# Performance work log

Hardware: AMD Instinct MI355X
Metric: run time of the kernel (lower is better)

The kernel has to match this reference:

```python
import jax, jax.numpy as jnp
import numpy as np

B, N, M = 64, 4096, 128
TOTAL_LABELS = 21
TOTAL_POS = 128
TOTAL_NEG = 128
VARIANCES = jnp.array([0.1, 0.1, 0.2, 0.2], dtype=jnp.float32)


def _make_boxes(key, b, n):
    # valid [y1, x1, y2, x2] boxes in [0, 1]
    k1, k2 = jax.random.split(key)
    c1 = jax.random.uniform(k1, (b, n, 2), dtype=jnp.float32)
    c2 = jax.random.uniform(k2, (b, n, 2), dtype=jnp.float32)
    lo = jnp.minimum(c1, c2)
    hi = jnp.maximum(c1, c2)
    return jnp.concatenate([lo, hi], axis=-1)


def setup_inputs() -> dict:
    key = jax.random.key(0)
    k1, k2, k3 = jax.random.split(key, 3)
    roi_bboxes = _make_boxes(k1, B, N)
    gt_boxes = _make_boxes(k2, B, M)
    gt_labels = jax.random.randint(k3, (B, M), 0, TOTAL_LABELS, dtype=jnp.int32)
    return {"roi_bboxes": roi_bboxes, "gt_boxes": gt_boxes, "gt_labels": gt_labels}


def generate_iou(bboxes, gt_boxes):
    # bboxes: [B,N,4], gt_boxes: [B,M,4]; format [y1,x1,y2,x2] -> iou [B,N,M]
    by1, bx1, by2, bx2 = jnp.split(bboxes, 4, axis=-1)      # each [B,N,1]
    gy1, gx1, gy2, gx2 = jnp.split(gt_boxes, 4, axis=-1)    # each [B,M,1]
    gt_area = ((gy2 - gy1) * (gx2 - gx1))[..., 0]           # [B,M]
    bbox_area = ((by2 - by1) * (bx2 - bx1))[..., 0]         # [B,N]
    x_top = jnp.maximum(bx1, jnp.swapaxes(gx1, 1, 2))       # [B,N,M]
    y_top = jnp.maximum(by1, jnp.swapaxes(gy1, 1, 2))
    x_bot = jnp.minimum(bx2, jnp.swapaxes(gx2, 1, 2))
    y_bot = jnp.minimum(by2, jnp.swapaxes(gy2, 1, 2))
    inter = jnp.maximum(x_bot - x_top, 0.0) * jnp.maximum(y_bot - y_top, 0.0)
    union = bbox_area[:, :, None] + gt_area[:, None, :] - inter
    return inter / union


def randomly_select_mask(key, mask, count):
    # keep at most `count` True entries per row, chosen at random (rpn_utils.randomly_select_xyz_mask)
    rand = jax.random.randint(key, mask.shape, 1, count * 10, dtype=jnp.int32)
    mult = mask.astype(jnp.int32) * rand
    order = jnp.argsort(-mult, axis=1)       # descending sort of masked random scores
    rank = jnp.argsort(order, axis=1)        # rank of each element in that order
    return mask & (rank < count)


def bbox_to_delta(bboxes, gt_boxes):
    bw = bboxes[..., 3] - bboxes[..., 1]
    bh = bboxes[..., 2] - bboxes[..., 0]
    bcx = bboxes[..., 1] + 0.5 * bw
    bcy = bboxes[..., 0] + 0.5 * bh
    gw = gt_boxes[..., 3] - gt_boxes[..., 1]
    gh = gt_boxes[..., 2] - gt_boxes[..., 0]
    gcx = gt_boxes[..., 1] + 0.5 * gw
    gcy = gt_boxes[..., 0] + 0.5 * gh
    bw = jnp.where(bw == 0.0, 1e-3, bw)
    bh = jnp.where(bh == 0.0, 1e-3, bh)
    dx = (gcx - bcx) / bw
    dy = (gcy - bcy) / bh
    gw_safe = jnp.where(gw == 0.0, 1.0, gw)  # avoid nan grads through masked log
    gh_safe = jnp.where(gh == 0.0, 1.0, gh)
    dw = jnp.where(gw == 0.0, 0.0, jnp.log(gw_safe / bw))
    dh = jnp.where(gh == 0.0, 0.0, jnp.log(gh_safe / bh))
    return jnp.stack([dy, dx, dh, dw], axis=-1)


def _forward(roi_bboxes, gt_boxes, gt_labels):
    kp, kn = jax.random.split(jax.random.key(42))
    iou_map = generate_iou(roi_bboxes, gt_boxes)             # [B,N,M]
    max_idx = jnp.argmax(iou_map, axis=2)                    # [B,N]
    merged = jnp.max(iou_map, axis=2)                        # [B,N]
    pos_mask = randomly_select_mask(kp, merged > 0.5, TOTAL_POS)
    neg_mask = randomly_select_mask(kn, (merged < 0.5) & (merged > 0.1), TOTAL_NEG)
    # batched gather of best-matching gt box / label per roi
    gt_boxes_map = jnp.take_along_axis(gt_boxes, max_idx[..., None], axis=1)   # [B,N,4]
    gt_labels_map = jnp.take_along_axis(gt_labels, max_idx, axis=1)            # [B,N]
    expanded_gt_boxes = jnp.where(pos_mask[..., None], gt_boxes_map, 0.0)
    pos_gt_labels = jnp.where(pos_mask, gt_labels_map, -1)
    expanded_gt_labels = pos_gt_labels  # hyper_params['background'] == False
    deltas = bbox_to_delta(roi_bboxes, expanded_gt_boxes) / VARIANCES           # [B,N,4]
    labels_oh = jax.nn.one_hot(expanded_gt_labels, TOTAL_LABELS, dtype=deltas.dtype)  # [B,N,L]; -1 -> all zeros
    roi_bbox_deltas = labels_oh[..., None] * deltas[..., None, :]               # [B,N,L,4]
    return roi_bbox_deltas, labels_oh


def reference(roi_bboxes, gt_boxes, gt_labels):
    return _forward(roi_bboxes, gt_boxes, gt_labels)
```

## Files before the change

### kernel.cpp

```cpp
#include <hip/hip_runtime.h>
#include <stdint.h>

#pragma clang fp contract(off)


#define BB 64
#define NN 4096
#define MM 128
#define LL 21
#define NTOT (BB * NN)
#define DELTA_ELEMS ((size_t)BB * NN * LL * 4)

__host__ __device__ __forceinline__ uint32_t rotl32(uint32_t v, int s) {
  return (v << s) | (v >> (32 - s));
}

__host__ __device__ inline void threefry2x32(uint32_t k0, uint32_t k1,
                                             uint32_t x0, uint32_t x1,
                                             uint32_t* o0, uint32_t* o1) {
  const uint32_t ks2 = k0 ^ k1 ^ 0x1BD11BDAu;
  x0 += k0; x1 += k1;
#define TF_R(r) do { x0 += x1; x1 = rotl32(x1, (r)); x1 ^= x0; } while (0)
  TF_R(13); TF_R(15); TF_R(26); TF_R(6);
  x0 += k1;  x1 += ks2 + 1u;
  TF_R(17); TF_R(29); TF_R(16); TF_R(24);
  x0 += ks2; x1 += k0 + 2u;
  TF_R(13); TF_R(15); TF_R(26); TF_R(6);
  x0 += k0;  x1 += k1 + 3u;
  TF_R(17); TF_R(29); TF_R(16); TF_R(24);
  x0 += k1;  x1 += ks2 + 4u;
  TF_R(13); TF_R(15); TF_R(26); TF_R(6);
  x0 += ks2; x1 += k0 + 5u;
#undef TF_R
  *o0 = x0; *o1 = x1;
}

__device__ __forceinline__ uint32_t jax_bits32(uint32_t ka, uint32_t kb, uint32_t idx) {
  uint32_t o0, o1;
  threefry2x32(ka, kb, 0u, idx, &o0, &o1);
  return o0 ^ o1;
}

__device__ __forceinline__ uint32_t jax_randint_1_1280(uint32_t k1a, uint32_t k1b,
                                                       uint32_t k2a, uint32_t k2b,
                                                       uint32_t idx) {
  const uint32_t hi = jax_bits32(k1a, k1b, idx);
  const uint32_t lo = jax_bits32(k2a, k2b, idx);
  const uint32_t off = ((hi % 1279u) * 882u + (lo % 1279u)) % 1279u;
  return 1u + off;
}

__device__ __forceinline__ float4 compute_delta(const float4 r, const float4 g) {
  float bh = r.z - r.x, bw = r.w - r.y;
  const float bcy = r.x + 0.5f * bh, bcx = r.y + 0.5f * bw;
  const float gh = g.z - g.x, gw = g.w - g.y;
  const float gcy = g.x + 0.5f * gh, gcx = g.y + 0.5f * gw;
  if (bw == 0.0f) bw = 1e-3f;
  if (bh == 0.0f) bh = 1e-3f;
  const float dx = (gcx - bcx) / bw;
  const float dy = (gcy - bcy) / bh;
  const float dw = (gw == 0.0f) ? 0.0f : logf(gw / bw);
  const float dh = (gh == 0.0f) ? 0.0f : logf(gh / bh);
  float4 dv;
  dv.x = dy / 0.1f; dv.y = dx / 0.1f; dv.z = dh / 0.2f; dv.w = dw / 0.2f;
  return dv;
}

__global__ __launch_bounds__(256) void iou_pack_kernel(
    const float* __restrict__ roi, const float* __restrict__ gt,
    uint32_t* __restrict__ packed,
    uint32_t k1a, uint32_t k1b, uint32_t k2a, uint32_t k2b) {
  __shared__ float4 gtb[MM];
  const int b = blockIdx.y;
  const int t = threadIdx.x;
  const int i = b * NN + blockIdx.x * 256 + t;
  const float4 r = ((const float4*)roi)[i];
  if (t < MM) gtb[t] = ((const float4*)gt)[b * MM + t];
  __syncthreads();
  const float barea = (r.z - r.x) * (r.w - r.y);
  float best = -1.0f;
  int bm = 0;
  #pragma unroll 4
  for (int m = 0; m < MM; ++m) {
    const float4 g = gtb[m];
    const float garea = (g.z - g.x) * (g.w - g.y);
    const float xt = fmaxf(r.y, g.y);
    const float yt = fmaxf(r.x, g.x);
    const float xb = fminf(r.w, g.w);
    const float yb = fminf(r.z, g.z);
    const float inter = fmaxf(xb - xt, 0.0f) * fmaxf(yb - yt, 0.0f);
    const float iou = inter / ((barea + garea) - inter);
    if (iou > best) { best = iou; bm = m; }
  }
  const uint32_t rnd = jax_randint_1_1280(k1a, k1b, k2a, k2b, (uint32_t)i);
  packed[i] = (uint32_t)bm | ((best > 0.5f) ? (rnd << 7) : 0u);
}

__global__ __launch_bounds__(256) void fused_out_kernel(
    const float* __restrict__ roi, const float* __restrict__ gt,
    const int* __restrict__ glab, const uint32_t* __restrict__ packed,
    float* __restrict__ out) {
  __shared__ uint32_t hist[1280];
  __shared__ uint32_t scan[257];
  __shared__ uint32_t wsum[4];
  __shared__ unsigned char selb[NN];
  __shared__ float4 sdv[256];
  __shared__ int slbl[256];
  __shared__ int s_thr;
  __shared__ int s_take;
  const int br = blockIdx.x;
  const int b = br >> 4;
  const int win0 = (br & 15) << 8;
  const int t = threadIdx.x;
  const int lane = t & 63;
  const int wid = t >> 6;

  const int irow = win0 + t;
  const int i = b * NN + irow;
  const uint32_t pk_own = packed[i];
  const uint4* p4 = (const uint4*)(packed + (size_t)b * NN);
  const uint4 w0 = p4[t * 4 + 0];
  const uint4 w1 = p4[t * 4 + 1];
  const uint4 w2 = p4[t * 4 + 2];
  const uint4 w3 = p4[t * 4 + 3];
  const float4 r = ((const float4*)roi)[i];

  for (int j = t; j < 1280; j += 256) hist[j] = 0u;
  if (t == 0) { s_thr = 0; s_take = 0; scan[256] = 0u; }
  __syncthreads();

  uint32_t rv[16];
  rv[0] = w0.x >> 7;  rv[1] = w0.y >> 7;  rv[2] = w0.z >> 7;  rv[3] = w0.w >> 7;
  rv[4] = w1.x >> 7;  rv[5] = w1.y >> 7;  rv[6] = w1.z >> 7;  rv[7] = w1.w >> 7;
  rv[8] = w2.x >> 7;  rv[9] = w2.y >> 7;  rv[10] = w2.z >> 7; rv[11] = w2.w >> 7;
  rv[12] = w3.x >> 7; rv[13] = w3.y >> 7; rv[14] = w3.z >> 7; rv[15] = w3.w >> 7;
  #pragma unroll
  for (int k = 0; k < 16; ++k)
    if (rv[k]) atomicAdd(&hist[rv[k]], 1u);

  const int mi = (int)(pk_own & 127u);
  const float4 g = ((const float4*)gt)[b * MM + mi];
  int lbl = glab[b * MM + mi];
  float4 dv = compute_delta(r, g);
  __syncthreads();

  uint32_t chunk = 0;
  #pragma unroll
  for (int j = 0; j < 5; ++j) chunk += hist[t * 5 + j];
  uint32_t v = chunk;
  #pragma unroll
  for (int off = 1; off < 64; off <<= 1) {
    const uint32_t u = __shfl_down(v, off);
    if (lane + off < 64) v += u;
  }
  if (lane == 0) wsum[wid] = v;
  __syncthreads();
  {
    uint32_t add = 0;
    #pragma unroll
    for (int w = 0; w < 4; ++w)
      if (w > wid) add += wsum[w];
    v += add;
  }
  scan[t] = v;
  __syncthreads();
  const uint32_t total = scan[0];
  if (total > 128u) {
    const uint32_t Sc = v;
    const uint32_t Sn = scan[t + 1];
    if (Sc >= 128u && Sn < 128u) {
      uint32_t s = Sn;
      #pragma unroll
      for (int j = 4; j >= 0; --j) {
        const uint32_t h = hist[t * 5 + j];
        if (s + h >= 128u) { s_thr = t * 5 + j; s_take = 128 - (int)s; break; }
        s += h;
      }
    }
  }
  __syncthreads();
  const uint32_t thr = (uint32_t)s_thr;
  const uint32_t take = (uint32_t)s_take;

  uint32_t lt = 0;
  if (thr > 0) {
    #pragma unroll
    for (int k = 0; k < 16; ++k) lt += (rv[k] == thr) ? 1u : 0u;
  }
  uint32_t p = lt;
  #pragma unroll
  for (int off = 1; off < 64; off <<= 1) {
    const uint32_t u = __shfl_up(p, off);
    if (lane >= off) p += u;
  }
  if (lane == 63) wsum[wid] = p;
  __syncthreads();
  uint32_t run = p - lt;
  #pragma unroll
  for (int w = 0; w < 4; ++w)
    if (w < wid) run += wsum[w];

  uint32_t sw0 = 0, sw1 = 0, sw2 = 0, sw3 = 0;
  #pragma unroll
  for (int k = 0; k < 16; ++k) {
    bool s;
    if (thr == 0) {
      s = rv[k] > 0u;
    } else {
      s = (rv[k] > thr);
      if (rv[k] == thr) { s = (run < take); ++run; }
    }
    const uint32_t bit = s ? 1u : 0u;
    if (k < 4)       sw0 |= bit << (k * 8);
    else if (k < 8)  sw1 |= bit << ((k - 4) * 8);
    else if (k < 12) sw2 |= bit << ((k - 8) * 8);
    else             sw3 |= bit << ((k - 12) * 8);
  }
  ((uint4*)selb)[t] = make_uint4(sw0, sw1, sw2, sw3);
  __syncthreads();

  if (!selb[irow]) lbl = -1;
  sdv[t] = dv;
  slbl[t] = lbl;
  __syncthreads();
  const float4 z = {0.f, 0.f, 0.f, 0.f};
  const size_t ri0 = (size_t)b * NN + win0;
  float4* dbase = (float4*)out + ri0 * LL;
  #pragma unroll
  for (int k = 0; k < LL; ++k) {
    const int q = t + k * 256;
    const int rr = q / 21;
    const int f = q - rr * 21;
    dbase[q] = (f == slbl[rr]) ? sdv[rr] : z;
  }
  float4* lbase = (float4*)(out + DELTA_ELEMS) + ri0 * LL / 4;
  for (int q = t; q < 1344; q += 256) {
    const int e0 = q * 4;
    float4 vv;
    const int r0 = e0 / 21;       vv.x = ((e0 - r0 * 21) == slbl[r0]) ? 1.f : 0.f;
    const int r1 = (e0 + 1) / 21; vv.y = ((e0 + 1 - r1 * 21) == slbl[r1]) ? 1.f : 0.f;
    const int r2 = (e0 + 2) / 21; vv.z = ((e0 + 2 - r2 * 21) == slbl[r2]) ? 1.f : 0.f;
    const int r3 = (e0 + 3) / 21; vv.w = ((e0 + 3 - r3 * 21) == slbl[r3]) ? 1.f : 0.f;
    lbase[q] = vv;
  }
}

__global__ __launch_bounds__(256) void iou_kernel_s(const float* __restrict__ roi,
                                                    const float* __restrict__ gt,
                                                    int* __restrict__ midx,
                                                    float* __restrict__ merged) {
  __shared__ float4 gtb[MM];
  const int b = blockIdx.y;
  const int t = threadIdx.x;
  if (t < MM) gtb[t] = ((const float4*)gt)[b * MM + t];
  __syncthreads();
  const int i = b * NN + blockIdx.x * 256 + t;
  const float4 r = ((const float4*)roi)[i];
  const float barea = (r.z - r.x) * (r.w - r.y);
  float best = -1.0f;
  int bm = 0;
  for (int m = 0; m < MM; ++m) {
    const float4 g = gtb[m];
    const float garea = (g.z - g.x) * (g.w - g.y);
    const float xt = fmaxf(r.y, g.y);
    const float yt = fmaxf(r.x, g.x);
    const float xb = fminf(r.w, g.w);
    const float yb = fminf(r.z, g.z);
    const float inter = fmaxf(xb - xt, 0.0f) * fmaxf(yb - yt, 0.0f);
    const float iou = inter / ((barea + garea) - inter);
    if (iou > best) { best = iou; bm = m; }
  }
  midx[(size_t)i * 84] = bm;
  merged[(size_t)i * 84] = best;
}

__global__ __launch_bounds__(256) void select_kernel_s(const float* __restrict__ merged,
                                                       int* __restrict__ sel,
                                                       uint32_t k1a, uint32_t k1b,
                                                       uint32_t k2a, uint32_t k2b) {
  __shared__ uint32_t buf[NN];
  __shared__ uint32_t hist[1280];
  __shared__ uint32_t scan[256];
  __shared__ int s_thr;
  __shared__ int s_take;
  const int b = blockIdx.x;
  const int t = threadIdx.x;
  for (int j = t; j < 1280; j += 256) hist[j] = 0u;
  if (t == 0) { s_thr = 0; s_take = 0; }
  #pragma unroll
  for (int k = 0; k < 16; ++k) {
    const int li = t + k * 256;
    buf[li] = __float_as_uint(merged[(size_t)(b * NN + li) * 84]);
  }
  __syncthreads();
  uint32_t rv[16];
  const int lbase = t * 16;
  #pragma unroll
  for (int k = 0; k < 16; ++k) {
    const int li = lbase + k;
    uint32_t r = 0u;
    if (__uint_as_float(buf[li]) > 0.5f) {
      r = jax_randint_1_1280(k1a, k1b, k2a, k2b, (uint32_t)(b * NN + li));
      atomicAdd(&hist[r], 1u);
    }
    rv[k] = r;
  }
  __syncthreads();
  uint32_t chunk = 0;
  #pragma unroll
  for (int j = 0; j < 5; ++j) chunk += hist[t * 5 + j];
  scan[t] = chunk;
  __syncthreads();
  for (int off = 1; off < 256; off <<= 1) {
    const uint32_t v = (t + off < 256) ? scan[t + off] : 0u;
    __syncthreads();
    scan[t] += v;
    __syncthreads();
  }
  const uint32_t total = scan[0];
  if (total > 128u) {
    const uint32_t Sc = scan[t];
    const uint32_t Sn = (t < 255) ? scan[t + 1] : 0u;
    if (Sc >= 128u && Sn < 128u) {
      uint32_t s = Sn;
      #pragma unroll
      for (int j = 4; j >= 0; --j) {
        const uint32_t h = hist[t * 5 + j];
        if (s + h >= 128u) { s_thr = t * 5 + j; s_take = 128 - (int)s; break; }
        s += h;
      }
    }
  }
  __syncthreads();
  const int thr = s_thr;
  const uint32_t take = (uint32_t)s_take;
  uint32_t lt = 0;
  if (thr > 0) {
    #pragma unroll
    for (int k = 0; k < 16; ++k) lt += (rv[k] == (uint32_t)thr) ? 1u : 0u;
  }
  scan[t] = lt;
  __syncthreads();
  for (int off = 1; off < 256; off <<= 1) {
    const uint32_t v = (t >= off) ? scan[t - off] : 0u;
    __syncthreads();
    scan[t] += v;
    __syncthreads();
  }
  uint32_t run = scan[t] - lt;
  #pragma unroll
  for (int k = 0; k < 16; ++k) {
    bool s;
    if (thr == 0) {
      s = rv[k] > 0u;
    } else {
      s = (rv[k] > (uint32_t)thr);
      if (rv[k] == (uint32_t)thr) { s = (run < take); ++run; }
    }
    buf[lbase + k] = s ? 1u : 0u;
  }
  __syncthreads();
  #pragma unroll
  for (int k = 0; k < 16; ++k) {
    const int li = t + k * 256;
    sel[(size_t)(b * NN + li) * 84] = (int)buf[li];
  }
}

__global__ __launch_bounds__(256) void out_kernel_s(const float* __restrict__ roi,
                                                    const float* __restrict__ gt,
                                                    const int* __restrict__ glab,
                                                    const int* __restrict__ midx,
                                                    const int* __restrict__ sel,
                                                    float* __restrict__ out) {
  __shared__ float4 sdv[256];
  __shared__ int slbl[256];
  const int t = threadIdx.x;
  const int ri0 = blockIdx.x * 256;
  const int i = ri0 + t;
  const int b = i >> 12;
  const int mi = midx[(size_t)i * 84];
  const int sv = sel[(size_t)i * 84];
  float4 dv = {0.f, 0.f, 0.f, 0.f};
  int lbl = -1;
  if (sv) {
    const float4 r = ((const float4*)roi)[i];
    const float4 g = ((const float4*)gt)[b * MM + mi];
    lbl = glab[b * MM + mi];
    dv = compute_delta(r, g);
  }
  sdv[t] = dv;
  slbl[t] = lbl;
  __syncthreads();
  const float4 z = {0.f, 0.f, 0.f, 0.f};
  float4* dbase = (float4*)out + (size_t)ri0 * LL;
  #pragma unroll
  for (int k = 0; k < LL; ++k) {
    const int q = t + k * 256;
    const int r = q / 21;
    const int f = q - r * 21;
    dbase[q] = (f == slbl[r]) ? sdv[r] : z;
  }
  float4* lbase = (float4*)(out + DELTA_ELEMS) + (size_t)ri0 * LL / 4;
  for (int q = t; q < 1344; q += 256) {
    const int e0 = q * 4;
    float4 v;
    const int r0 = e0 / 21;       v.x = ((e0 - r0 * 21) == slbl[r0]) ? 1.f : 0.f;
    const int r1 = (e0 + 1) / 21; v.y = ((e0 + 1 - r1 * 21) == slbl[r1]) ? 1.f : 0.f;
    const int r2 = (e0 + 2) / 21; v.z = ((e0 + 2 - r2 * 21) == slbl[r2]) ? 1.f : 0.f;
    const int r3 = (e0 + 3) / 21; v.w = ((e0 + 3 - r3 * 21) == slbl[r3]) ? 1.f : 0.f;
    lbase[q] = v;
  }
}

extern "C" void kernel_launch(void* const* d_in, const int* in_sizes, int n_in,
                              void* d_out, int out_size, void* d_ws, size_t ws_size,
                              hipStream_t stream) {
  const float* roi = (const float*)d_in[0];
  const float* gt  = (const float*)d_in[1];
  const int* glab  = (const int*)d_in[2];
  float* out = (float*)d_out;

  uint32_t kp0, kp1, k1a, k1b, k2a, k2b;
  threefry2x32(0u, 42u, 0u, 0u, &kp0, &kp1);
  threefry2x32(kp0, kp1, 0u, 0u, &k1a, &k1b);
  threefry2x32(kp0, kp1, 0u, 1u, &k2a, &k2b);

  if (d_ws != nullptr && ws_size >= (size_t)NTOT * 4) {
    uint32_t* packed = (uint32_t*)d_ws;
    hipLaunchKernelGGL(iou_pack_kernel, dim3(NN / 256, BB), dim3(256), 0, stream,
                       roi, gt, packed, k1a, k1b, k2a, k2b);
    hipLaunchKernelGGL(fused_out_kernel, dim3(NTOT / 256), dim3(256), 0, stream,
                       roi, gt, glab, packed, out);
  } else {
    int* midx     = (int*)out;
    float* merged = out + 1;
    int* sel      = (int*)out + 2;
    hipLaunchKernelGGL(iou_kernel_s, dim3(NN / 256, BB), dim3(256), 0, stream,
                       roi, gt, midx, merged);
    hipLaunchKernelGGL(select_kernel_s, dim3(BB), dim3(256), 0, stream,
                       merged, sel, k1a, k1b, k2a, k2b);
    hipLaunchKernelGGL(out_kernel_s, dim3(NTOT / 256), dim3(256), 0, stream,
                       roi, gt, glab, midx, sel, out);
  }
}
```

Measured before the change: 57.58 us.

## Fuse IoU-pack and output kernels into one persistent kernel with grid barrier

Replaces the two-launch pipeline (IoU/pack kernel, then selection/output kernel) with a single 512-block kernel in which each thread processes two ROIs. Blocks synchronise through a software grid barrier built on an atomic counter in the workspace, so the packed per-batch scores are visible to all blocks before the histogram-based selection. Each block now covers 512 rows, which halves how many times the per-batch histogram and scan are recomputed, and removes the inter-kernel launch gap. It relies on all 512 blocks being co-resident (launch_bounds 256,2). The spin loop has a timeout guard that could silently break the barrier and produce wrong results if blocks are not all resident.

Measured after the change: 112.4 us. 1.95x slower.

```diff
diff --git a/kernel.cpp b/kernel.cpp
--- a/kernel.cpp
+++ b/kernel.cpp
@@ -10,6 +10,7 @@
 #define LL 21
 #define NTOT (BB * NN)
 #define DELTA_ELEMS ((size_t)BB * NN * LL * 4)
+#define NBLK 512
 
 __host__ __device__ __forceinline__ uint32_t rotl32(uint32_t v, int s) {
   return (v << s) | (v >> (32 - s));
@@ -66,64 +67,97 @@
   return dv;
 }
 
-__global__ __launch_bounds__(256) void iou_pack_kernel(
+__global__ __launch_bounds__(256, 2) void mega_kernel(
     const float* __restrict__ roi, const float* __restrict__ gt,
-    uint32_t* __restrict__ packed,
+    const int* __restrict__ glab, uint32_t* __restrict__ packed,
+    uint32_t* __restrict__ barA, const uint32_t* __restrict__ barB,
+    float* __restrict__ out,
     uint32_t k1a, uint32_t k1b, uint32_t k2a, uint32_t k2b) {
   __shared__ float4 gtb[MM];
-  const int b = blockIdx.y;
+  __shared__ uint32_t hist[1280];
+  __shared__ uint32_t scan[257];
+  __shared__ uint32_t wsum[4];
+  __shared__ unsigned char selb[512];
+  __shared__ float4 sdv[256];
+  __shared__ int slbl[256];
+  __shared__ int s_thr;
+  __shared__ int s_take;
+
+  const int br = blockIdx.x;
+  const int b = br >> 3;
+  const int wbase = (br & 7) << 9;
   const int t = threadIdx.x;
-  const int i = b * NN + blockIdx.x * 256 + t;
-  const float4 r = ((const float4*)roi)[i];
+  const int lane = t & 63;
+  const int wid = t >> 6;
+
+  const int i0 = b * NN + wbase + t;
+  const int i1 = i0 + 256;
+  const float4 r0 = ((const float4*)roi)[i0];
+  const float4 r1 = ((const float4*)roi)[i1];
   if (t < MM) gtb[t] = ((const float4*)gt)[b * MM + t];
   __syncthreads();
-  const float barea = (r.z - r.x) * (r.w - r.y);
-  float best = -1.0f;
-  int bm = 0;
+  const float ba0 = (r0.z - r0.x) * (r0.w - r0.y);
+  const float ba1 = (r1.z - r1.x) * (r1.w - r1.y);
+  float best0 = -1.0f, best1 = -1.0f;
+  int bm0 = 0, bm1 = 0;
   #pragma unroll 4
   for (int m = 0; m < MM; ++m) {
     const float4 g = gtb[m];
     const float garea = (g.z - g.x) * (g.w - g.y);
-    const float xt = fmaxf(r.y, g.y);
-    const float yt = fmaxf(r.x, g.x);
-    const float xb = fminf(r.w, g.w);
-    const float yb = fminf(r.z, g.z);
-    const float inter = fmaxf(xb - xt, 0.0f) * fmaxf(yb - yt, 0.0f);
-    const float iou = inter / ((barea + garea) - inter);
-    if (iou > best) { best = iou; bm = m; }
-  }
-  const uint32_t rnd = jax_randint_1_1280(k1a, k1b, k2a, k2b, (uint32_t)i);
-  packed[i] = (uint32_t)bm | ((best > 0.5f) ? (rnd << 7) : 0u);
-}
-
-__global__ __launch_bounds__(256) void fused_out_kernel(
-    const float* __restrict__ roi, const float* __restrict__ gt,
-    const int* __restrict__ glab, const uint32_t* __restrict__ packed,
-    float* __restrict__ out) {
-  __shared__ uint32_t hist[1280];
-  __shared__ uint32_t scan[257];
-  __shared__ uint32_t wsum[4];
-  __shared__ unsigned char selb[NN];
-  __shared__ float4 sdv[256];
-  __shared__ int slbl[256];
-  __shared__ int s_thr;
-  __shared__ int s_take;
-  const int br = blockIdx.x;
-  const int b = br >> 4;
-  const int win0 = (br & 15) << 8;
-  const int t = threadIdx.x;
-  const int lane = t & 63;
-  const int wid = t >> 6;
-
-  const int irow = win0 + t;
-  const int i = b * NN + irow;
-  const uint32_t pk_own = packed[i];
+    {
+      const float xt = fmaxf(r0.y, g.y);
+      const float yt = fmaxf(r0.x, g.x);
+      const float xb = fminf(r0.w, g.w);
+      const float yb = fminf(r0.z, g.z);
+      const float inter = fmaxf(xb - xt, 0.0f) * fmaxf(yb - yt, 0.0f);
+      const float iou = inter / ((ba0 + garea) - inter);
+      if (iou > best0) { best0 = iou; bm0 = m; }
+    }
+    {
+      const float xt = fmaxf(r1.y, g.y);
+      const float yt = fmaxf(r1.x, g.x);
+      const float xb = fminf(r1.w, g.w);
+      const float yb = fminf(r1.z, g.z);
+      const float inter = fmaxf(xb - xt, 0.0f) * fmaxf(yb - yt, 0.0f);
+      const float iou = inter / ((ba1 + garea) - inter);
+      if (iou > best1) { best1 = iou; bm1 = m; }
+    }
+  }
+  const uint32_t rnd0 = jax_randint_1_1280(k1a, k1b, k2a, k2b, (uint32_t)i0);
+  const uint32_t rnd1 = jax_randint_1_1280(k1a, k1b, k2a, k2b, (uint32_t)i1);
+  const uint32_t pk0 = (uint32_t)bm0 | ((best0 > 0.5f) ? (rnd0 << 7) : 0u);
+  const uint32_t pk1 = (uint32_t)bm1 | ((best1 > 0.5f) ? (rnd1 << 7) : 0u);
+  packed[i0] = pk0;
+  packed[i1] = pk1;
+
+  __syncthreads();
+  if (t == 0) {
+    const uint32_t base = __hip_atomic_load((uint32_t*)barB, __ATOMIC_RELAXED,
+                                            __HIP_MEMORY_SCOPE_AGENT);
+    const uint32_t old = __hip_atomic_fetch_add(barA, 1u, __ATOMIC_RELEASE,
+                                                __HIP_MEMORY_SCOPE_AGENT);
+    const uint32_t target = base + ((((old - base) >> 9) + 1u) << 9);
+    int guard = 0;
+    while ((int32_t)(__hip_atomic_load(barA, __ATOMIC_ACQUIRE,
+                                       __HIP_MEMORY_SCOPE_AGENT) - target) < 0) {
+      __builtin_amdgcn_s_sleep(2);
+      if (++guard > (1 << 21)) break;
+    }
+  }
+  __syncthreads();
+  __threadfence();
+
+  const int mi0 = (int)(pk0 & 127u);
+  const int mi1 = (int)(pk1 & 127u);
+  const int lbl0g = glab[b * MM + mi0];
+  const int lbl1g = glab[b * MM + mi1];
   const uint4* p4 = (const uint4*)(packed + (size_t)b * NN);
   const uint4 w0 = p4[t * 4 + 0];
   const uint4 w1 = p4[t * 4 + 1];
   const uint4 w2 = p4[t * 4 + 2];
   const uint4 w3 = p4[t * 4 + 3];
-  const float4 r = ((const float4*)roi)[i];
+  const float4 dv0 = compute_delta(r0, gtb[mi0]);
+  const float4 dv1 = compute_delta(r1, gtb[mi1]);
 
   for (int j = t; j < 1280; j += 256) hist[j] = 0u;
   if (t == 0) { s_thr = 0; s_take = 0; scan[256] = 0u; }
@@ -137,11 +171,6 @@
   #pragma unroll
   for (int k = 0; k < 16; ++k)
     if (rv[k]) atomicAdd(&hist[rv[k]], 1u);
-
-  const int mi = (int)(pk_own & 127u);
-  const float4 g = ((const float4*)gt)[b * MM + mi];
-  int lbl = glab[b * MM + mi];
-  float4 dv = compute_delta(r, g);
   __syncthreads();
 
   uint32_t chunk = 0;
@@ -200,7 +229,8 @@
   for (int w = 0; w < 4; ++w)
     if (w < wid) run += wsum[w];
 
-  uint32_t sw0 = 0, sw1 = 0, sw2 = 0, sw3 = 0;
+  const int ownerlo = wbase >> 4;
+  const bool owner = (t >= ownerlo) && (t < ownerlo + 32);
   #pragma unroll
   for (int k = 0; k < 16; ++k) {
     bool s;
@@ -210,38 +240,59 @@
       s = (rv[k] > thr);
       if (rv[k] == thr) { s = (run < take); ++run; }
     }
-    const uint32_t bit = s ? 1u : 0u;
-    if (k < 4)       sw0 |= bit << (k * 8);
-    else if (k < 8)  sw1 |= bit << ((k - 4) * 8);
-    else if (k < 12) sw2 |= bit << ((k - 8) * 8);
-    else             sw3 |= bit << ((k - 12) * 8);
-  }
-  ((uint4*)selb)[t] = make_uint4(sw0, sw1, sw2, sw3);
-  __syncthreads();
-
-  if (!selb[irow]) lbl = -1;
-  sdv[t] = dv;
-  slbl[t] = lbl;
-  __syncthreads();
+    if (owner) selb[(t - ownerlo) * 16 + k] = s ? 1 : 0;
+  }
+  __syncthreads();
+
   const float4 z = {0.f, 0.f, 0.f, 0.f};
-  const size_t ri0 = (size_t)b * NN + win0;
-  float4* dbase = (float4*)out + ri0 * LL;
-  #pragma unroll
-  for (int k = 0; k < LL; ++k) {
-    const int q = t + k * 256;
-    const int rr = q / 21;
-    const int f = q - rr * 21;
-    dbase[q] = (f == slbl[rr]) ? sdv[rr] : z;
-  }
-  float4* lbase = (float4*)(out + DELTA_ELEMS) + ri0 * LL / 4;
-  for (int q = t; q < 1344; q += 256) {
-    const int e0 = q * 4;
-    float4 vv;
-    const int r0 = e0 / 21;       vv.x = ((e0 - r0 * 21) == slbl[r0]) ? 1.f : 0.f;
-    const int r1 = (e0 + 1) / 21; vv.y = ((e0 + 1 - r1 * 21) == slbl[r1]) ? 1.f : 0.f;
-    const int r2 = (e0 + 2) / 21; vv.z = ((e0 + 2 - r2 * 21) == slbl[r2]) ? 1.f : 0.f;
-    const int r3 = (e0 + 3) / 21; vv.w = ((e0 + 3 - r3 * 21) == slbl[r3]) ? 1.f : 0.f;
-    lbase[q] = vv;
+  sdv[t] = dv0;
+  slbl[t] = selb[t] ? lbl0g : -1;
+  __syncthreads();
+  {
+    const size_t ri0 = (size_t)b * NN + wbase;
+    float4* dbase = (float4*)out + ri0 * LL;
+    #pragma unroll
+    for (int k = 0; k < LL; ++k) {
+      const int q = t + k * 256;
+      const int rr = q / 21;
+      const int f = q - rr * 21;
+      dbase[q] = (f == slbl[rr]) ? sdv[rr] : z;
+    }
+    float4* lbase = (float4*)(out + DELTA_ELEMS) + ri0 * LL / 4;
+    for (int q = t; q < 1344; q += 256) {
+      const int e0 = q * 4;
+      float4 vv;
+      const int r0i = e0 / 21;       vv.x = ((e0 - r0i * 21) == slbl[r0i]) ? 1.f : 0.f;
+      const int r1i = (e0 + 1) / 21; vv.y = ((e0 + 1 - r1i * 21) == slbl[r1i]) ? 1.f : 0.f;
+      const int r2i = (e0 + 2) / 21; vv.z = ((e0 + 2 - r2i * 21) == slbl[r2i]) ? 1.f : 0.f;
+      const int r3i = (e0 + 3) / 21; vv.w = ((e0 + 3 - r3i * 21) == slbl[r3i]) ? 1.f : 0.f;
+      lbase[q] = vv;
+    }
+  }
+  __syncthreads();
+  sdv[t] = dv1;
+  slbl[t] = selb[256 + t] ? lbl1g : -1;
+  __syncthreads();
+  {
+    const size_t ri0 = (size_t)b * NN + wbase + 256;
+    float4* dbase = (float4*)out + ri0 * LL;
+    #pragma unroll
+    for (int k = 0; k < LL; ++k) {
+      const int q = t + k * 256;
+      const int rr = q / 21;
+      const int f = q - rr * 21;
+      dbase[q] = (f == slbl[rr]) ? sdv[rr] : z;
+    }
+    float4* lbase = (float4*)(out + DELTA_ELEMS) + ri0 * LL / 4;
+    for (int q = t; q < 1344; q += 256) {
+      const int e0 = q * 4;
+      float4 vv;
+      const int r0i = e0 / 21;       vv.x = ((e0 - r0i * 21) == slbl[r0i]) ? 1.f : 0.f;
+      const int r1i = (e0 + 1) / 21; vv.y = ((e0 + 1 - r1i * 21) == slbl[r1i]) ? 1.f : 0.f;
+      const int r2i = (e0 + 2) / 21; vv.z = ((e0 + 2 - r2i * 21) == slbl[r2i]) ? 1.f : 0.f;
+      const int r3i = (e0 + 3) / 21; vv.w = ((e0 + 3 - r3i * 21) == slbl[r3i]) ? 1.f : 0.f;
+      lbase[q] = vv;
+    }
   }
 }
 
@@ -426,12 +477,13 @@
   threefry2x32(kp0, kp1, 0u, 0u, &k1a, &k1b);
   threefry2x32(kp0, kp1, 0u, 1u, &k2a, &k2b);
 
-  if (d_ws != nullptr && ws_size >= (size_t)NTOT * 4) {
+  if (d_ws != nullptr && ws_size >= (size_t)NTOT * 4 + 256) {
     uint32_t* packed = (uint32_t*)d_ws;
-    hipLaunchKernelGGL(iou_pack_kernel, dim3(NN / 256, BB), dim3(256), 0, stream,
-                       roi, gt, packed, k1a, k1b, k2a, k2b);
-    hipLaunchKernelGGL(fused_out_kernel, dim3(NTOT / 256), dim3(256), 0, stream,
-                       roi, gt, glab, packed, out);
+    uint32_t* barA = (uint32_t*)((char*)d_ws + (size_t)NTOT * 4);
+    uint32_t* barB = barA + 32;
+    hipLaunchKernelGGL(mega_kernel, dim3(NBLK), dim3(256), 0, stream,
+                       roi, gt, glab, packed, barA, barB, out,
+                       k1a, k1b, k2a, k2b);
   } else {
     int* midx     = (int*)out;
     float* merged = out + 1;
```
